# Optimization experiments

Measured on AMD Instinct MI355X. Metric: run time of the kernel, lower is better.

The kernel has to match this reference:

```python
import jax, jax.numpy as jnp
import numpy as np

H = 4      # attention heads
C = 64     # hidden_dim per head
GAT_SLOPE = 0.2   # PyG GATConv leaky_relu negative_slope
ACT_SLOPE = 0.01  # nn.LeakyReLU / F.leaky_relu default


def gat_layer(x, src, dst, W, a_src, a_dst, b, n):
    # x: [n, F_in] -> h: [n, H, C]
    h = (x @ W).reshape(n, H, C)
    al_s = jnp.einsum('nhc,hc->nh', h, a_src)  # [n, H]
    al_d = jnp.einsum('nhc,hc->nh', h, a_dst)
    e = jax.nn.leaky_relu(al_s[src] + al_d[dst], GAT_SLOPE)  # [E, H]
    # segment softmax over destination nodes (self-loops ensure non-empty segments)
    m = jax.ops.segment_max(e, dst, num_segments=n)
    p = jnp.exp(e - m[dst])
    s = jax.ops.segment_sum(p, dst, num_segments=n)
    alpha = p / s[dst]
    out = jax.ops.segment_sum(h[src] * alpha[:, :, None], dst, num_segments=n)  # [n, H, C]
    return out.reshape(n, H * C) + b


def setup_inputs() -> dict:
    key = jax.random.key(0)
    ks = jax.random.split(key, 24)
    N, E = 102400, 409600
    F_IN, F_OUT = 80, 80
    HC = H * C
    RIN, RHID, ROUT = 60, 512, 60
    def g(k, shape, scale):
        return (jax.random.normal(k, shape, dtype=jnp.float32) * scale)
    inp = {
        'x': g(ks[0], (N, F_IN), 1.0),
        'edge_index': jax.random.randint(ks[1], (2, E), 0, N, dtype=jnp.int64),
        'root_ctx_norm': g(ks[2], (4096, RIN), 1.0),
        'W0': g(ks[3], (F_IN, HC), 0.1), 'a_src0': g(ks[4], (H, C), 0.1), 'a_dst0': g(ks[5], (H, C), 0.1), 'b0': jnp.zeros((HC,), jnp.float32),
        'W1': g(ks[6], (HC, HC), 0.06), 'a_src1': g(ks[7], (H, C), 0.1), 'a_dst1': g(ks[8], (H, C), 0.1), 'b1': jnp.zeros((HC,), jnp.float32),
        'W2': g(ks[9], (HC, HC), 0.06), 'a_src2': g(ks[10], (H, C), 0.1), 'a_dst2': g(ks[11], (H, C), 0.1), 'b2': jnp.zeros((HC,), jnp.float32),
        'fc_w': g(ks[12], (HC, F_OUT), 0.06), 'fc_b': jnp.zeros((F_OUT,), jnp.float32),
        'r_w1': g(ks[13], (RIN, RHID), 0.1), 'r_b1': jnp.zeros((RHID,), jnp.float32),
        'r_w2': g(ks[14], (RHID, RHID), 0.04), 'r_b2': jnp.zeros((RHID,), jnp.float32),
        'r_w3': g(ks[15], (RHID, ROUT), 0.04), 'r_b3': jnp.zeros((ROUT,), jnp.float32),
    }
    return inp


def reference(x, edge_index, root_ctx_norm,
              W0, a_src0, a_dst0, b0,
              W1, a_src1, a_dst1, b1,
              W2, a_src2, a_dst2, b2,
              fc_w, fc_b, r_w1, r_b1, r_w2, r_b2, r_w3, r_b3):
    n = x.shape[0]
    loops = jnp.arange(n, dtype=edge_index.dtype)
    src = jnp.concatenate([edge_index[0], loops])  # PyG add_self_loops=True
    dst = jnp.concatenate([edge_index[1], loops])
    h = gat_layer(x, src, dst, W0, a_src0, a_dst0, b0, n)
    h = jax.nn.leaky_relu(h, ACT_SLOPE)  # dropout is identity in eval
    h = gat_layer(h, src, dst, W1, a_src1, a_dst1, b1, n)
    h = jax.nn.leaky_relu(h, ACT_SLOPE)
    h = gat_layer(h, src, dst, W2, a_src2, a_dst2, b2, n)
    rot = h @ fc_w + fc_b
    r = jax.nn.leaky_relu(root_ctx_norm @ r_w1 + r_b1, ACT_SLOPE)
    r = jax.nn.leaky_relu(r @ r_w2 + r_b2, ACT_SLOPE)
    root_norm = r @ r_w3 + r_b3
    return rot, root_norm
```

## Files before the change

kernel.cpp:

```cpp
#include <hip/hip_runtime.h>
#include <hip/hip_bf16.h>


#define GAT_SLOPE 0.2f
#define ACT_SLOPE 0.01f

typedef unsigned short ushort_t;
typedef __attribute__((ext_vector_type(8))) short bf16x8;
typedef __attribute__((ext_vector_type(8))) unsigned short ushort8v;
typedef __attribute__((ext_vector_type(4))) unsigned short ushort4v;
typedef __attribute__((ext_vector_type(4))) float floatx4;

__device__ __forceinline__ float lrelu(float x, float s) {
    return fmaxf(x, s * x);
}

__device__ __forceinline__ ushort_t f2bf(float f) {
    union { float f; unsigned u; } x; x.f = f;
    unsigned r = x.u + 0x7FFF + ((x.u >> 16) & 1);
    return (ushort_t)(r >> 16);
}

__device__ __forceinline__ float bf2f(ushort_t u) {
    union { unsigned u; float f; } x; x.u = ((unsigned)u) << 16;
    return x.f;
}

__device__ __forceinline__ void gl_lds16(const ushort_t* g, ushort_t* l) {
    __builtin_amdgcn_global_load_lds(
        (const __attribute__((address_space(1))) unsigned int*)g,
        (__attribute__((address_space(3))) unsigned int*)l, 16, 0, 0);
}

__global__ void detect_fmt(const int* __restrict__ raw, int nwords, int* flag) {
    __shared__ int nz;
    if (threadIdx.x == 0) nz = 0;
    __syncthreads();
    int lim = nwords < 4096 ? nwords : 4096;
    for (int i = threadIdx.x * 2 + 1; i < lim; i += 512)
        if (raw[i] != 0) atomicAdd(&nz, 1);
    __syncthreads();
    if (threadIdx.x == 0) *flag = (nz == 0) ? 1 : 0;
}

__global__ void zero2(int* __restrict__ a, int* __restrict__ b, int n) {
    int i = blockIdx.x * blockDim.x + threadIdx.x;
    if (i < n) { a[i] = 0; b[i] = 0; }
}

__global__ void convert_count(const int* __restrict__ raw, int E,
                              const int* __restrict__ flag,
                              int* __restrict__ idx32, int* __restrict__ counts) {
    int i = blockIdx.x * blockDim.x + threadIdx.x;
    if (i >= E) return;
    int f = *flag;
    int s = f ? raw[2 * i] : raw[i];
    int d = f ? raw[2 * (E + i)] : raw[E + i];
    idx32[i] = s;
    idx32[E + i] = d;
    atomicAdd(&counts[d], 1);
}

__global__ void scan_block(const int* __restrict__ counts, int* __restrict__ inc,
                           int* __restrict__ blockSums, int N) {
    __shared__ int sh[256];
    int i = blockIdx.x * 256 + threadIdx.x;
    int v = (i < N) ? counts[i] : 0;
    sh[threadIdx.x] = v;
    __syncthreads();
    for (int off = 1; off < 256; off <<= 1) {
        int t = (threadIdx.x >= off) ? sh[threadIdx.x - off] : 0;
        __syncthreads();
        sh[threadIdx.x] += t;
        __syncthreads();
    }
    if (i < N) inc[i] = sh[threadIdx.x];
    if (threadIdx.x == 255) blockSums[blockIdx.x] = sh[255];
}

__global__ void scan_sums(int* __restrict__ blockSums, int nb, int* __restrict__ row_ptr) {
    __shared__ int sh[512];
    int v = ((int)threadIdx.x < nb) ? blockSums[threadIdx.x] : 0;
    sh[threadIdx.x] = v;
    __syncthreads();
    for (int off = 1; off < 512; off <<= 1) {
        int t = (threadIdx.x >= off) ? sh[threadIdx.x - off] : 0;
        __syncthreads();
        sh[threadIdx.x] += t;
        __syncthreads();
    }
    if ((int)threadIdx.x < nb) blockSums[threadIdx.x] = sh[threadIdx.x];
    if (threadIdx.x == 0) row_ptr[0] = 0;
}

__global__ void scan_add(const int* __restrict__ inc, const int* __restrict__ blockSums,
                         int* __restrict__ row_ptr, int N) {
    int i = blockIdx.x * 256 + threadIdx.x;
    if (i < N) row_ptr[i + 1] = inc[i] + (blockIdx.x > 0 ? blockSums[blockIdx.x - 1] : 0);
}

__global__ void edge_fill(const int* __restrict__ src, const int* __restrict__ dst, int E,
                          const int* __restrict__ row_ptr, int* __restrict__ cursor,
                          int* __restrict__ col) {
    int i = blockIdx.x * blockDim.x + threadIdx.x;
    if (i < E) {
        int d = dst[i];
        int pos = row_ptr[d] + atomicAdd(&cursor[d], 1);
        col[pos] = src[i];
    }
}

__global__ void convert_padrow(const float* __restrict__ in, ushort_t* __restrict__ out,
                               int M, int Kr, int Kp) {
    int i = blockIdx.x * blockDim.x + threadIdx.x;
    if (i >= M * Kp) return;
    int r = i / Kp, c = i - r * Kp;
    out[i] = f2bf((c < Kr) ? in[(size_t)r * Kr + c] : 0.f);
}

struct WConv { const float* in; ushort_t* out; int Kp, Kr, N, Npad, blkOff; };
struct WConvArr { WConv e[7]; int n; };

__global__ void convert_w_multi(WConvArr a) {
    int b = blockIdx.x;
    int ei = 0;
    for (int k = 1; k < a.n; k++)
        if (b >= a.e[k].blkOff) ei = k;
    WConv w = a.e[ei];
    int i = (b - w.blkOff) * 256 + threadIdx.x;
    if (i >= w.Npad * w.Kp) return;
    int n = i / w.Kp, k = i - n * w.Kp;
    float v = (n < w.N && k < w.Kr) ? w.in[(size_t)k * w.N + n] : 0.f;
    w.out[i] = f2bf(v);
}

__global__ __launch_bounds__(256) void gemm_gat(
    const ushort_t* __restrict__ A, const ushort_t* __restrict__ Bt,
    const float* __restrict__ a_src, const float* __restrict__ a_dst,
    ushort_t* __restrict__ Hbf, float* __restrict__ al_s, float* __restrict__ al_d,
    int M, int K) {
    __shared__ __align__(16) ushort_t As[128 * 32];
    __shared__ __align__(16) ushort_t Bs[128 * 32];
    int t = threadIdx.x;
    int wave = t >> 6, lane = t & 63;
    int wm = (wave >> 1) << 6;
    int wn = (wave & 1) << 6;
    int rowBase = blockIdx.y << 7;
    int colBase = blockIdx.x << 7;
    int lrow = lane & 15, lquad = lane >> 4;
    floatx4 acc[4][4];
#pragma unroll
    for (int i = 0; i < 4; i++)
#pragma unroll
        for (int j = 0; j < 4; j++) acc[i][j] = (floatx4){0.f, 0.f, 0.f, 0.f};

    int c0 = wave * 64 + lane;
    const ushort_t* gA0 = A + (size_t)(rowBase + (c0 >> 2)) * K + ((c0 & 3) << 3);
    const ushort_t* gB0 = Bt + (size_t)(colBase + (c0 >> 2)) * K + ((c0 & 3) << 3);
    int c1 = 256 + c0;
    const ushort_t* gA1 = A + (size_t)(rowBase + (c1 >> 2)) * K + ((c1 & 3) << 3);
    const ushort_t* gB1 = Bt + (size_t)(colBase + (c1 >> 2)) * K + ((c1 & 3) << 3);
    ushort_t* lA0 = As + (size_t)(wave * 64) * 8;
    ushort_t* lB0 = Bs + (size_t)(wave * 64) * 8;
    ushort_t* lA1 = As + (size_t)(256 + wave * 64) * 8;
    ushort_t* lB1 = Bs + (size_t)(256 + wave * 64) * 8;

    for (int k0 = 0; k0 < K; k0 += 32) {
        gl_lds16(gA0 + k0, lA0);
        gl_lds16(gA1 + k0, lA1);
        gl_lds16(gB0 + k0, lB0);
        gl_lds16(gB1 + k0, lB1);
        __syncthreads();
        bf16x8 af[4], bfv[4];
#pragma unroll
        for (int i = 0; i < 4; i++)
            af[i] = *(const bf16x8*)(As + (wm + i * 16 + lrow) * 32 + lquad * 8);
#pragma unroll
        for (int j = 0; j < 4; j++)
            bfv[j] = *(const bf16x8*)(Bs + (wn + j * 16 + lrow) * 32 + lquad * 8);
#pragma unroll
        for (int i = 0; i < 4; i++)
#pragma unroll
            for (int j = 0; j < 4; j++)
                acc[i][j] = __builtin_amdgcn_mfma_f32_16x16x32_bf16(af[i], bfv[j],
                                                                    acc[i][j], 0, 0, 0);
        __syncthreads();
    }
    int head = (colBase + wn) >> 6;
    float avs[4], avd[4];
#pragma unroll
    for (int j = 0; j < 4; j++) {
        avs[j] = a_src[head * 64 + j * 16 + lrow];
        avd[j] = a_dst[head * 64 + j * 16 + lrow];
    }
#pragma unroll
    for (int i = 0; i < 4; i++) {
#pragma unroll
        for (int r = 0; r < 4; r++) {
            float ps = 0.f, pd = 0.f;
#pragma unroll
            for (int j = 0; j < 4; j++) {
                ps += acc[i][j][r] * avs[j];
                pd += acc[i][j][r] * avd[j];
            }
#pragma unroll
            for (int off = 1; off < 16; off <<= 1) {
                ps += __shfl_xor(ps, off);
                pd += __shfl_xor(pd, off);
            }
            if (lrow == 0) {
                int gr = rowBase + wm + i * 16 + lquad * 4 + r;
                al_s[gr * 4 + head] = ps;
                al_d[gr * 4 + head] = pd;
            }
        }
        int grb = rowBase + wm + i * 16 + lquad * 4;
#pragma unroll
        for (int j = 0; j < 4; j++) {
            int gc = colBase + wn + j * 16 + lrow;
#pragma unroll
            for (int r = 0; r < 4; r++)
                Hbf[(size_t)(grb + r) * 256 + gc] = f2bf(acc[i][j][r]);
        }
    }
}

__global__ __launch_bounds__(256) void gemm_plain(
    const ushort_t* __restrict__ A, const ushort_t* __restrict__ Bt,
    const float* __restrict__ bias, void* __restrict__ Cout,
    int M, int N, int K, int act, float slope, int outBf) {
    __shared__ __align__(16) ushort_t As[128 * 32];
    __shared__ __align__(16) ushort_t Bs[128 * 32];
    int t = threadIdx.x;
    int wave = t >> 6, lane = t & 63;
    int wm = (wave >> 1) << 6;
    int wn = (wave & 1) << 6;
    int rowBase = blockIdx.y << 7;
    int colBase = blockIdx.x << 7;
    int lrow = lane & 15, lquad = lane >> 4;
    floatx4 acc[4][4];
#pragma unroll
    for (int i = 0; i < 4; i++)
#pragma unroll
        for (int j = 0; j < 4; j++) acc[i][j] = (floatx4){0.f, 0.f, 0.f, 0.f};

    int c0 = wave * 64 + lane;
    const ushort_t* gA0 = A + (size_t)(rowBase + (c0 >> 2)) * K + ((c0 & 3) << 3);
    const ushort_t* gB0 = Bt + (size_t)(colBase + (c0 >> 2)) * K + ((c0 & 3) << 3);
    int c1 = 256 + c0;
    const ushort_t* gA1 = A + (size_t)(rowBase + (c1 >> 2)) * K + ((c1 & 3) << 3);
    const ushort_t* gB1 = Bt + (size_t)(colBase + (c1 >> 2)) * K + ((c1 & 3) << 3);
    ushort_t* lA0 = As + (size_t)(wave * 64) * 8;
    ushort_t* lB0 = Bs + (size_t)(wave * 64) * 8;
    ushort_t* lA1 = As + (size_t)(256 + wave * 64) * 8;
    ushort_t* lB1 = Bs + (size_t)(256 + wave * 64) * 8;

    for (int k0 = 0; k0 < K; k0 += 32) {
        gl_lds16(gA0 + k0, lA0);
        gl_lds16(gA1 + k0, lA1);
        gl_lds16(gB0 + k0, lB0);
        gl_lds16(gB1 + k0, lB1);
        __syncthreads();
        bf16x8 af[4], bfv[4];
#pragma unroll
        for (int i = 0; i < 4; i++)
            af[i] = *(const bf16x8*)(As + (wm + i * 16 + lrow) * 32 + lquad * 8);
#pragma unroll
        for (int j = 0; j < 4; j++)
            bfv[j] = *(const bf16x8*)(Bs + (wn + j * 16 + lrow) * 32 + lquad * 8);
#pragma unroll
        for (int i = 0; i < 4; i++)
#pragma unroll
            for (int j = 0; j < 4; j++)
                acc[i][j] = __builtin_amdgcn_mfma_f32_16x16x32_bf16(af[i], bfv[j],
                                                                    acc[i][j], 0, 0, 0);
        __syncthreads();
    }
#pragma unroll
    for (int i = 0; i < 4; i++) {
        int gr = rowBase + wm + i * 16 + lquad * 4;
#pragma unroll
        for (int j = 0; j < 4; j++) {
            int gc = colBase + wn + j * 16 + lrow;
            if (gc >= N) continue;
            float b = bias ? bias[gc] : 0.f;
#pragma unroll
            for (int r = 0; r < 4; r++) {
                float v = acc[i][j][r] + b;
                if (act) v = lrelu(v, slope);
                if (outBf)
                    ((ushort_t*)Cout)[(size_t)(gr + r) * N + gc] = f2bf(v);
                else
                    ((float*)Cout)[(size_t)(gr + r) * N + gc] = v;
            }
        }
    }
}

__global__ __launch_bounds__(256) void gat_agg(
    const ushort_t* __restrict__ h_bf, const float* __restrict__ al_s,
    const float* __restrict__ al_d, const int* __restrict__ row_ptr,
    const int* __restrict__ col, const float* __restrict__ bias,
    ushort_t* __restrict__ out_bf, int N, int act, float slope) {
    int wid = (blockIdx.x * 256 + threadIdx.x) >> 6;
    int lane = threadIdx.x & 63;
    int half = lane >> 5;
    int lane8 = lane & 31;
    int n = wid * 2 + half;
    if (n >= N) return;
    int head = lane8 >> 3;
    int idx4 = n * 4 + head;
    float ad = al_d[idx4];
    const ushort8v* h8 = (const ushort8v*)h_bf;
    float p = __expf(lrelu(al_s[idx4] + ad, GAT_SLOPE));
    ushort8v hv = h8[(size_t)n * 32 + lane8];
    float s = p;
    float acc[8];
#pragma unroll
    for (int c = 0; c < 8; c++) acc[c] = p * bf2f(hv[c]);
    int beg = row_ptr[n], end = row_ptr[n + 1];
    for (int i = beg; i < end; i += 4) {
        int cnt = end - i;
        int sn0 = col[i];
        int sn1 = (cnt > 1) ? col[i + 1] : sn0;
        int sn2 = (cnt > 2) ? col[i + 2] : sn0;
        int sn3 = (cnt > 3) ? col[i + 3] : sn0;
        ushort8v h0 = h8[(size_t)sn0 * 32 + lane8];
        ushort8v h1 = h8[(size_t)sn1 * 32 + lane8];
        ushort8v h2 = h8[(size_t)sn2 * 32 + lane8];
        ushort8v h3 = h8[(size_t)sn3 * 32 + lane8];
        float a0 = al_s[sn0 * 4 + head];
        float a1 = al_s[sn1 * 4 + head];
        float a2 = al_s[sn2 * 4 + head];
        float a3 = al_s[sn3 * 4 + head];
        float p0 = __expf(lrelu(a0 + ad, GAT_SLOPE));
#pragma unroll
        for (int c = 0; c < 8; c++) acc[c] += p0 * bf2f(h0[c]);
        s += p0;
        if (cnt > 1) {
            float p1 = __expf(lrelu(a1 + ad, GAT_SLOPE));
#pragma unroll
            for (int c = 0; c < 8; c++) acc[c] += p1 * bf2f(h1[c]);
            s += p1;
        }
        if (cnt > 2) {
            float p2 = __expf(lrelu(a2 + ad, GAT_SLOPE));
#pragma unroll
            for (int c = 0; c < 8; c++) acc[c] += p2 * bf2f(h2[c]);
            s += p2;
        }
        if (cnt > 3) {
            float p3 = __expf(lrelu(a3 + ad, GAT_SLOPE));
#pragma unroll
            for (int c = 0; c < 8; c++) acc[c] += p3 * bf2f(h3[c]);
            s += p3;
        }
    }
    float rs = 1.f / s;
    const float4* b4 = (const float4*)bias;
    float4 b0 = b4[lane8 * 2];
    float4 b1 = b4[lane8 * 2 + 1];
    float bv[8] = {b0.x, b0.y, b0.z, b0.w, b1.x, b1.y, b1.z, b1.w};
    ushort8v o;
#pragma unroll
    for (int c = 0; c < 8; c++) {
        float v = acc[c] * rs + bv[c];
        if (act) v = lrelu(v, slope);
        o[c] = f2bf(v);
    }
    ((ushort8v*)out_bf)[(size_t)n * 32 + lane8] = o;
}

extern "C" void kernel_launch(void* const* d_in, const int* in_sizes, int n_in,
                              void* d_out, int out_size, void* d_ws, size_t ws_size,
                              hipStream_t stream) {
    const float* x        = (const float*)d_in[0];
    const int*   rawEdge  = (const int*)d_in[1];
    const float* rootCtx  = (const float*)d_in[2];
    const float* W[3]     = {(const float*)d_in[3], (const float*)d_in[7], (const float*)d_in[11]};
    const float* aS[3]    = {(const float*)d_in[4], (const float*)d_in[8], (const float*)d_in[12]};
    const float* aD[3]    = {(const float*)d_in[5], (const float*)d_in[9], (const float*)d_in[13]};
    const float* bb[3]    = {(const float*)d_in[6], (const float*)d_in[10], (const float*)d_in[14]};
    const float* fc_w     = (const float*)d_in[15];
    const float* fc_b     = (const float*)d_in[16];
    const float* r_w1     = (const float*)d_in[17];
    const float* r_b1     = (const float*)d_in[18];
    const float* r_w2     = (const float*)d_in[19];
    const float* r_b2     = (const float*)d_in[20];
    const float* r_w3     = (const float*)d_in[21];
    const float* r_b3     = (const float*)d_in[22];

    const int N  = in_sizes[0] / 80;
    const int E  = in_sizes[1] / 2;
    const int R  = in_sizes[2] / 60;
    const int N4 = N * 4;

    float* outRot  = (float*)d_out;
    float* outRoot = (float*)d_out + (size_t)N * 80;

    size_t off = 0;
    auto carve = [&](size_t bytes) -> void* {
        off = (off + 255) & ~(size_t)255;
        void* p = (char*)d_ws + off;
        off += bytes;
        return p;
    };
    int*      flag      = (int*)carve(4);
    int*      idx32     = (int*)carve((size_t)2 * E * 4);
    int*      counts    = (int*)carve((size_t)N * 4);
    int*      cursor    = (int*)carve((size_t)N * 4);
    int*      row_ptr   = (int*)carve((size_t)(N + 1) * 4);
    int*      incArr    = (int*)carve((size_t)N * 4);
    int*      blockSums = (int*)carve(512 * 4);
    int*      colArr    = (int*)carve((size_t)E * 4);
    float*    al_s      = (float*)carve((size_t)N4 * 4);
    float*    al_d      = (float*)carve((size_t)N4 * 4);
    ushort_t* h_bf      = (ushort_t*)carve((size_t)N * 256 * 2);
    ushort_t* agg_bf    = (ushort_t*)carve((size_t)N * 256 * 2);
    ushort_t* x_bf      = (ushort_t*)carve((size_t)N * 96 * 2);
    ushort_t* rc_bf     = (ushort_t*)carve((size_t)R * 64 * 2);
    ushort_t* t1_bf     = (ushort_t*)carve((size_t)R * 512 * 2);
    ushort_t* t2_bf     = (ushort_t*)carve((size_t)R * 512 * 2);
    ushort_t* Wt0       = (ushort_t*)carve((size_t)256 * 96 * 2);
    ushort_t* Wt1       = (ushort_t*)carve((size_t)256 * 256 * 2);
    ushort_t* Wt2       = (ushort_t*)carve((size_t)256 * 256 * 2);
    ushort_t* fcWt      = (ushort_t*)carve((size_t)128 * 256 * 2);
    ushort_t* rW1t      = (ushort_t*)carve((size_t)512 * 64 * 2);
    ushort_t* rWt2      = (ushort_t*)carve((size_t)512 * 512 * 2);
    ushort_t* rWt3      = (ushort_t*)carve((size_t)128 * 512 * 2);

    const int nb = (N + 255) / 256;
    dim3 blk(256);

    detect_fmt<<<1, 256, 0, stream>>>(rawEdge, 2 * E, flag);
    zero2<<<(N + 255) / 256, blk, 0, stream>>>(counts, cursor, N);
    convert_count<<<(E + 255) / 256, blk, 0, stream>>>(rawEdge, E, flag, idx32, counts);
    const int* srcArr = idx32;
    const int* dstArr = idx32 + E;
    scan_block<<<nb, 256, 0, stream>>>(counts, incArr, blockSums, N);
    scan_sums<<<1, 512, 0, stream>>>(blockSums, nb, row_ptr);
    scan_add<<<nb, 256, 0, stream>>>(incArr, blockSums, row_ptr, N);
    edge_fill<<<(E + 255) / 256, blk, 0, stream>>>(srcArr, dstArr, E, row_ptr, cursor, colArr);

    {
        WConvArr wa;
        auto mk = [&](int i, const float* in, ushort_t* out, int Kp, int Kr, int Nn, int Npad,
                      int blkOff) {
            wa.e[i] = WConv{in, out, Kp, Kr, Nn, Npad, blkOff};
        };
        int boff = 0;
        auto nblk = [](int Npad, int Kp) { return (Npad * Kp + 255) / 256; };
        mk(0, W[0], Wt0, 96, 80, 256, 256, boff);   boff += nblk(256, 96);
        mk(1, W[1], Wt1, 256, 256, 256, 256, boff); boff += nblk(256, 256);
        mk(2, W[2], Wt2, 256, 256, 256, 256, boff); boff += nblk(256, 256);
        mk(3, fc_w, fcWt, 256, 256, 80, 128, boff); boff += nblk(128, 256);
        mk(4, r_w1, rW1t, 64, 60, 512, 512, boff);  boff += nblk(512, 64);
        mk(5, r_w2, rWt2, 512, 512, 512, 512, boff); boff += nblk(512, 512);
        mk(6, r_w3, rWt3, 512, 512, 60, 128, boff);  boff += nblk(128, 512);
        wa.n = 7;
        convert_w_multi<<<boff, blk, 0, stream>>>(wa);
    }
    convert_padrow<<<(N * 96 + 255) / 256, blk, 0, stream>>>(x, x_bf, N, 80, 96);
    convert_padrow<<<(R * 64 + 255) / 256, blk, 0, stream>>>(rootCtx, rc_bf, R, 60, 64);

    const int aggBlocks = (N / 2 + 3) / 4;
    const ushort_t* curA = x_bf;
    int curK = 96;
    for (int l = 0; l < 3; l++) {
        dim3 g1(2, N / 128);
        gemm_gat<<<g1, blk, 0, stream>>>(curA, l == 0 ? Wt0 : (l == 1 ? Wt1 : Wt2),
                                         aS[l], aD[l], h_bf, al_s, al_d, N, curK);
        int act = (l < 2) ? 1 : 0;
        gat_agg<<<aggBlocks, blk, 0, stream>>>(h_bf, al_s, al_d, row_ptr,
                                               colArr, bb[l], agg_bf, N,
                                               act, ACT_SLOPE);
        curA = agg_bf;
        curK = 256;
    }

    {
        dim3 g(1, N / 128);
        gemm_plain<<<g, blk, 0, stream>>>(agg_bf, fcWt, fc_b, outRot, N, 80, 256,
                                          0, 0.f, 0);
    }
    {
        dim3 g1(512 / 128, R / 128);
        gemm_plain<<<g1, blk, 0, stream>>>(rc_bf, rW1t, r_b1, t1_bf, R, 512, 64,
                                           1, ACT_SLOPE, 1);
        dim3 g2(512 / 128, R / 128);
        gemm_plain<<<g2, blk, 0, stream>>>(t1_bf, rWt2, r_b2, t2_bf, R, 512, 512,
                                           1, ACT_SLOPE, 1);
        dim3 g3(1, R / 128);
        gemm_plain<<<g3, blk, 0, stream>>>(t2_bf, rWt3, r_b3, outRoot, R, 60, 512,
                                           0, 0.f, 0);
    }
}
```

Measured before the change: 520.8 us.

## Double-buffer LDS tiles in both GEMM kernels to overlap loads with MFMA

```diff
diff --git a/kernel.cpp b/kernel.cpp
--- a/kernel.cpp
+++ b/kernel.cpp
@@ -139,8 +139,8 @@
     const float* __restrict__ a_src, const float* __restrict__ a_dst,
     ushort_t* __restrict__ Hbf, float* __restrict__ al_s, float* __restrict__ al_d,
     int M, int K) {
-    __shared__ __align__(16) ushort_t As[128 * 32];
-    __shared__ __align__(16) ushort_t Bs[128 * 32];
+    __shared__ __align__(16) ushort_t As[2][128 * 32];
+    __shared__ __align__(16) ushort_t Bs[2][128 * 32];
     int t = threadIdx.x;
     int wave = t >> 6, lane = t & 63;
     int wm = (wave >> 1) << 6;
@@ -160,32 +160,53 @@
     int c1 = 256 + c0;
     const ushort_t* gA1 = A + (size_t)(rowBase + (c1 >> 2)) * K + ((c1 & 3) << 3);
     const ushort_t* gB1 = Bt + (size_t)(colBase + (c1 >> 2)) * K + ((c1 & 3) << 3);
-    ushort_t* lA0 = As + (size_t)(wave * 64) * 8;
-    ushort_t* lB0 = Bs + (size_t)(wave * 64) * 8;
-    ushort_t* lA1 = As + (size_t)(256 + wave * 64) * 8;
-    ushort_t* lB1 = Bs + (size_t)(256 + wave * 64) * 8;
-
-    for (int k0 = 0; k0 < K; k0 += 32) {
-        gl_lds16(gA0 + k0, lA0);
-        gl_lds16(gA1 + k0, lA1);
-        gl_lds16(gB0 + k0, lB0);
-        gl_lds16(gB1 + k0, lB1);
-        __syncthreads();
+    const int ldsOff0 = (wave * 64) * 8;
+    const int ldsOff1 = (256 + wave * 64) * 8;
+
+    const int nt = K >> 5;
+#define STAGE_GAT(tt, b)                          \
+    do {                                          \
+        int k0_ = (tt) << 5;                      \
+        gl_lds16(gA0 + k0_, &As[b][ldsOff0]);     \
+        gl_lds16(gA1 + k0_, &As[b][ldsOff1]);     \
+        gl_lds16(gB0 + k0_, &Bs[b][ldsOff0]);     \
+        gl_lds16(gB1 + k0_, &Bs[b][ldsOff1]);     \
+    } while (0)
+
+    STAGE_GAT(0, 0);
+    STAGE_GAT(1, 1);
+    asm volatile("s_waitcnt vmcnt(4)" ::: "memory");
+    __builtin_amdgcn_s_barrier();
+
+    for (int kt = 0; kt < nt; ++kt) {
+        int b = kt & 1;
         bf16x8 af[4], bfv[4];
 #pragma unroll
         for (int i = 0; i < 4; i++)
-            af[i] = *(const bf16x8*)(As + (wm + i * 16 + lrow) * 32 + lquad * 8);
+            af[i] = *(const bf16x8*)(&As[b][(wm + i * 16 + lrow) * 32 + lquad * 8]);
 #pragma unroll
         for (int j = 0; j < 4; j++)
-            bfv[j] = *(const bf16x8*)(Bs + (wn + j * 16 + lrow) * 32 + lquad * 8);
+            bfv[j] = *(const bf16x8*)(&Bs[b][(wn + j * 16 + lrow) * 32 + lquad * 8]);
+        asm volatile("s_waitcnt lgkmcnt(0)" ::: "memory");
+        __builtin_amdgcn_sched_barrier(0);
+        __builtin_amdgcn_s_barrier();
+        bool more = (kt + 2) < nt;
+        if (more) STAGE_GAT(kt + 2, b);
 #pragma unroll
         for (int i = 0; i < 4; i++)
 #pragma unroll
             for (int j = 0; j < 4; j++)
                 acc[i][j] = __builtin_amdgcn_mfma_f32_16x16x32_bf16(af[i], bfv[j],
                                                                     acc[i][j], 0, 0, 0);
-        __syncthreads();
-    }
+        if (more)
+            asm volatile("s_waitcnt vmcnt(4)" ::: "memory");
+        else
+            asm volatile("s_waitcnt vmcnt(0)" ::: "memory");
+        __builtin_amdgcn_s_barrier();
+        __builtin_amdgcn_sched_barrier(0);
+    }
+#undef STAGE_GAT
+
     int head = (colBase + wn) >> 6;
     float avs[4], avd[4];
 #pragma unroll
@@ -229,8 +250,8 @@
     const ushort_t* __restrict__ A, const ushort_t* __restrict__ Bt,
     const float* __restrict__ bias, void* __restrict__ Cout,
     int M, int N, int K, int act, float slope, int outBf) {
-    __shared__ __align__(16) ushort_t As[128 * 32];
-    __shared__ __align__(16) ushort_t Bs[128 * 32];
+    __shared__ __align__(16) ushort_t As[2][128 * 32];
+    __shared__ __align__(16) ushort_t Bs[2][128 * 32];
     int t = threadIdx.x;
     int wave = t >> 6, lane = t & 63;
     int wm = (wave >> 1) << 6;
@@ -250,32 +271,53 @@
     int c1 = 256 + c0;
     const ushort_t* gA1 = A + (size_t)(rowBase + (c1 >> 2)) * K + ((c1 & 3) << 3);
     const ushort_t* gB1 = Bt + (size_t)(colBase + (c1 >> 2)) * K + ((c1 & 3) << 3);
-    ushort_t* lA0 = As + (size_t)(wave * 64) * 8;
-    ushort_t* lB0 = Bs + (size_t)(wave * 64) * 8;
-    ushort_t* lA1 = As + (size_t)(256 + wave * 64) * 8;
-    ushort_t* lB1 = Bs + (size_t)(256 + wave * 64) * 8;
-
-    for (int k0 = 0; k0 < K; k0 += 32) {
-        gl_lds16(gA0 + k0, lA0);
-        gl_lds16(gA1 + k0, lA1);
-        gl_lds16(gB0 + k0, lB0);
-        gl_lds16(gB1 + k0, lB1);
-        __syncthreads();
+    const int ldsOff0 = (wave * 64) * 8;
+    const int ldsOff1 = (256 + wave * 64) * 8;
+
+    const int nt = K >> 5;
+#define STAGE_PLN(tt, b)                          \
+    do {                                          \
+        int k0_ = (tt) << 5;                      \
+        gl_lds16(gA0 + k0_, &As[b][ldsOff0]);     \
+        gl_lds16(gA1 + k0_, &As[b][ldsOff1]);     \
+        gl_lds16(gB0 + k0_, &Bs[b][ldsOff0]);     \
+        gl_lds16(gB1 + k0_, &Bs[b][ldsOff1]);     \
+    } while (0)
+
+    STAGE_PLN(0, 0);
+    STAGE_PLN(1, 1);
+    asm volatile("s_waitcnt vmcnt(4)" ::: "memory");
+    __builtin_amdgcn_s_barrier();
+
+    for (int kt = 0; kt < nt; ++kt) {
+        int b = kt & 1;
         bf16x8 af[4], bfv[4];
 #pragma unroll
         for (int i = 0; i < 4; i++)
-            af[i] = *(const bf16x8*)(As + (wm + i * 16 + lrow) * 32 + lquad * 8);
+            af[i] = *(const bf16x8*)(&As[b][(wm + i * 16 + lrow) * 32 + lquad * 8]);
 #pragma unroll
         for (int j = 0; j < 4; j++)
-            bfv[j] = *(const bf16x8*)(Bs + (wn + j * 16 + lrow) * 32 + lquad * 8);
+            bfv[j] = *(const bf16x8*)(&Bs[b][(wn + j * 16 + lrow) * 32 + lquad * 8]);
+        asm volatile("s_waitcnt lgkmcnt(0)" ::: "memory");
+        __builtin_amdgcn_sched_barrier(0);
+        __builtin_amdgcn_s_barrier();
+        bool more = (kt + 2) < nt;
+        if (more) STAGE_PLN(kt + 2, b);
 #pragma unroll
         for (int i = 0; i < 4; i++)
 #pragma unroll
             for (int j = 0; j < 4; j++)
                 acc[i][j] = __builtin_amdgcn_mfma_f32_16x16x32_bf16(af[i], bfv[j],
                                                                     acc[i][j], 0, 0, 0);
-        __syncthreads();
-    }
+        if (more)
+            asm volatile("s_waitcnt vmcnt(4)" ::: "memory");
+        else
+            asm volatile("s_waitcnt vmcnt(0)" ::: "memory");
+        __builtin_amdgcn_s_barrier();
+        __builtin_amdgcn_sched_barrier(0);
+    }
+#undef STAGE_PLN
+
 #pragma unroll
     for (int i = 0; i < 4; i++) {
         int gr = rowBase + wm + i * 16 + lquad * 4;
```

After: 514.8 us. Within noise of the previous version (-1.2%).

## Double-buffer GEMM tiles with register-staged prefetch and 64-wide K steps

Applied to the files above, without the earlier changes.

```diff
diff --git a/kernel.cpp b/kernel.cpp
--- a/kernel.cpp
+++ b/kernel.cpp
@@ -8,7 +8,6 @@
 typedef unsigned short ushort_t;
 typedef __attribute__((ext_vector_type(8))) short bf16x8;
 typedef __attribute__((ext_vector_type(8))) unsigned short ushort8v;
-typedef __attribute__((ext_vector_type(4))) unsigned short ushort4v;
 typedef __attribute__((ext_vector_type(4))) float floatx4;
 
 __device__ __forceinline__ float lrelu(float x, float s) {
@@ -24,12 +23,6 @@
 __device__ __forceinline__ float bf2f(ushort_t u) {
     union { unsigned u; float f; } x; x.u = ((unsigned)u) << 16;
     return x.f;
-}
-
-__device__ __forceinline__ void gl_lds16(const ushort_t* g, ushort_t* l) {
-    __builtin_amdgcn_global_load_lds(
-        (const __attribute__((address_space(1))) unsigned int*)g,
-        (__attribute__((address_space(3))) unsigned int*)l, 16, 0, 0);
 }
 
 __global__ void detect_fmt(const int* __restrict__ raw, int nwords, int* flag) {
@@ -134,13 +127,60 @@
     w.out[i] = f2bf(v);
 }
 
+#define DECL_P()                                      \
+    ushort8v pa0, pa1, pb0, pb1, qa0, qa1, qb0, qb1
+
+#define LOADP(pp)                                     \
+    do {                                              \
+        int k0_ = (pp) << 6;                          \
+        pa0 = *(const ushort8v*)(gA0 + k0_);          \
+        pa1 = *(const ushort8v*)(gA1 + k0_);          \
+        pb0 = *(const ushort8v*)(gB0 + k0_);          \
+        pb1 = *(const ushort8v*)(gB1 + k0_);          \
+        qa0 = *(const ushort8v*)(gA0 + k0_ + 32);     \
+        qa1 = *(const ushort8v*)(gA1 + k0_ + 32);     \
+        qb0 = *(const ushort8v*)(gB0 + k0_ + 32);     \
+        qb1 = *(const ushort8v*)(gB1 + k0_ + 32);     \
+    } while (0)
+
+#define WRITEP(b)                                     \
+    do {                                              \
+        *(ushort8v*)(&As[b][wsl0]) = pa0;             \
+        *(ushort8v*)(&As[b][wsl1]) = pa1;             \
+        *(ushort8v*)(&Bs[b][wsl0]) = pb0;             \
+        *(ushort8v*)(&Bs[b][wsl1]) = pb1;             \
+        *(ushort8v*)(&As[b][4096 + wsl0]) = qa0;      \
+        *(ushort8v*)(&As[b][4096 + wsl1]) = qa1;      \
+        *(ushort8v*)(&Bs[b][4096 + wsl0]) = qb0;      \
+        *(ushort8v*)(&Bs[b][4096 + wsl1]) = qb1;      \
+    } while (0)
+
+#define MFMA_SUB(b, base)                                                        \
+    do {                                                                         \
+        bf16x8 af[4], bfv[4];                                                    \
+        _Pragma("unroll")                                                        \
+        for (int i = 0; i < 4; i++)                                              \
+            af[i] = *(const bf16x8*)(&As[b][(base) + (wm + i * 16 + lrow) * 32   \
+                                            + lquad * 8]);                       \
+        _Pragma("unroll")                                                        \
+        for (int j = 0; j < 4; j++)                                              \
+            bfv[j] = *(const bf16x8*)(&Bs[b][(base) + (wn + j * 16 + lrow) * 32  \
+                                             + lquad * 8]);                      \
+        _Pragma("unroll")                                                        \
+        for (int i = 0; i < 4; i++)                                              \
+            _Pragma("unroll")                                                    \
+            for (int j = 0; j < 4; j++)                                          \
+                acc[i][j] = __builtin_amdgcn_mfma_f32_16x16x32_bf16(             \
+                    af[i], bfv[j], acc[i][j], 0, 0, 0);                          \
+    } while (0)
+
 __global__ __launch_bounds__(256) void gemm_gat(
     const ushort_t* __restrict__ A, const ushort_t* __restrict__ Bt,
     const float* __restrict__ a_src, const float* __restrict__ a_dst,
     ushort_t* __restrict__ Hbf, float* __restrict__ al_s, float* __restrict__ al_d,
     int M, int K) {
-    __shared__ __align__(16) ushort_t As[128 * 32];
-    __shared__ __align__(16) ushort_t Bs[128 * 32];
+    __shared__ __align__(16) ushort_t As[2][128 * 64];
+    __shared__ __align__(16) ushort_t Bs[2][128 * 64];
     int t = threadIdx.x;
     int wave = t >> 6, lane = t & 63;
     int wm = (wave >> 1) << 6;
@@ -160,32 +200,28 @@
     int c1 = 256 + c0;
     const ushort_t* gA1 = A + (size_t)(rowBase + (c1 >> 2)) * K + ((c1 & 3) << 3);
     const ushort_t* gB1 = Bt + (size_t)(colBase + (c1 >> 2)) * K + ((c1 & 3) << 3);
-    ushort_t* lA0 = As + (size_t)(wave * 64) * 8;
-    ushort_t* lB0 = Bs + (size_t)(wave * 64) * 8;
-    ushort_t* lA1 = As + (size_t)(256 + wave * 64) * 8;
-    ushort_t* lB1 = Bs + (size_t)(256 + wave * 64) * 8;
-
-    for (int k0 = 0; k0 < K; k0 += 32) {
-        gl_lds16(gA0 + k0, lA0);
-        gl_lds16(gA1 + k0, lA1);
-        gl_lds16(gB0 + k0, lB0);
-        gl_lds16(gB1 + k0, lB1);
-        __syncthreads();
-        bf16x8 af[4], bfv[4];
-#pragma unroll
-        for (int i = 0; i < 4; i++)
-            af[i] = *(const bf16x8*)(As + (wm + i * 16 + lrow) * 32 + lquad * 8);
-#pragma unroll
-        for (int j = 0; j < 4; j++)
-            bfv[j] = *(const bf16x8*)(Bs + (wn + j * 16 + lrow) * 32 + lquad * 8);
-#pragma unroll
-        for (int i = 0; i < 4; i++)
-#pragma unroll
-            for (int j = 0; j < 4; j++)
-                acc[i][j] = __builtin_amdgcn_mfma_f32_16x16x32_bf16(af[i], bfv[j],
-                                                                    acc[i][j], 0, 0, 0);
-        __syncthreads();
-    }
+    const int wsl0 = (wave * 64 + lane) * 8;
+    const int wsl1 = (256 + wave * 64 + lane) * 8;
+
+    const int np = K >> 6;
+    DECL_P();
+
+    LOADP(0);
+    WRITEP(0);
+    if (np > 1) LOADP(1);
+    asm volatile("s_waitcnt lgkmcnt(0)" ::: "memory");
+    __builtin_amdgcn_s_barrier();
+
+    for (int kp = 0; kp < np; ++kp) {
+        int b = kp & 1;
+        if (kp + 1 < np) WRITEP(b ^ 1);
+        if (kp + 2 < np) LOADP(kp + 2);
+        MFMA_SUB(b, 0);
+        MFMA_SUB(b, 4096);
+        asm volatile("s_waitcnt lgkmcnt(0)" ::: "memory");
+        __builtin_amdgcn_s_barrier();
+    }
+
     int head = (colBase + wn) >> 6;
     float avs[4], avd[4];
 #pragma unroll
@@ -229,8 +265,8 @@
     const ushort_t* __restrict__ A, const ushort_t* __restrict__ Bt,
     const float* __restrict__ bias, void* __restrict__ Cout,
     int M, int N, int K, int act, float slope, int outBf) {
-    __shared__ __align__(16) ushort_t As[128 * 32];
-    __shared__ __align__(16) ushort_t Bs[128 * 32];
+    __shared__ __align__(16) ushort_t As[2][128 * 64];
+    __shared__ __align__(16) ushort_t Bs[2][128 * 64];
     int t = threadIdx.x;
     int wave = t >> 6, lane = t & 63;
     int wm = (wave >> 1) << 6;
@@ -250,32 +286,28 @@
     int c1 = 256 + c0;
     const ushort_t* gA1 = A + (size_t)(rowBase + (c1 >> 2)) * K + ((c1 & 3) << 3);
     const ushort_t* gB1 = Bt + (size_t)(colBase + (c1 >> 2)) * K + ((c1 & 3) << 3);
-    ushort_t* lA0 = As + (size_t)(wave * 64) * 8;
-    ushort_t* lB0 = Bs + (size_t)(wave * 64) * 8;
-    ushort_t* lA1 = As + (size_t)(256 + wave * 64) * 8;
-    ushort_t* lB1 = Bs + (size_t)(256 + wave * 64) * 8;
-
-    for (int k0 = 0; k0 < K; k0 += 32) {
-        gl_lds16(gA0 + k0, lA0);
-        gl_lds16(gA1 + k0, lA1);
-        gl_lds16(gB0 + k0, lB0);
-        gl_lds16(gB1 + k0, lB1);
-        __syncthreads();
-        bf16x8 af[4], bfv[4];
-#pragma unroll
-        for (int i = 0; i < 4; i++)
-            af[i] = *(const bf16x8*)(As + (wm + i * 16 + lrow) * 32 + lquad * 8);
-#pragma unroll
-        for (int j = 0; j < 4; j++)
-            bfv[j] = *(const bf16x8*)(Bs + (wn + j * 16 + lrow) * 32 + lquad * 8);
-#pragma unroll
-        for (int i = 0; i < 4; i++)
-#pragma unroll
-            for (int j = 0; j < 4; j++)
-                acc[i][j] = __builtin_amdgcn_mfma_f32_16x16x32_bf16(af[i], bfv[j],
-                                                                    acc[i][j], 0, 0, 0);
-        __syncthreads();
-    }
+    const int wsl0 = (wave * 64 + lane) * 8;
+    const int wsl1 = (256 + wave * 64 + lane) * 8;
+
+    const int np = K >> 6;
+    DECL_P();
+
+    LOADP(0);
+    WRITEP(0);
+    if (np > 1) LOADP(1);
+    asm volatile("s_waitcnt lgkmcnt(0)" ::: "memory");
+    __builtin_amdgcn_s_barrier();
+
+    for (int kp = 0; kp < np; ++kp) {
+        int b = kp & 1;
+        if (kp + 1 < np) WRITEP(b ^ 1);
+        if (kp + 2 < np) LOADP(kp + 2);
+        MFMA_SUB(b, 0);
+        MFMA_SUB(b, 4096);
+        asm volatile("s_waitcnt lgkmcnt(0)" ::: "memory");
+        __builtin_amdgcn_s_barrier();
+    }
+
 #pragma unroll
     for (int i = 0; i < 4; i++) {
         int gr = rowBase + wm + i * 16 + lquad * 4;
@@ -417,11 +449,11 @@
     float*    al_d      = (float*)carve((size_t)N4 * 4);
     ushort_t* h_bf      = (ushort_t*)carve((size_t)N * 256 * 2);
     ushort_t* agg_bf    = (ushort_t*)carve((size_t)N * 256 * 2);
-    ushort_t* x_bf      = (ushort_t*)carve((size_t)N * 96 * 2);
+    ushort_t* x_bf      = (ushort_t*)carve((size_t)N * 128 * 2);
     ushort_t* rc_bf     = (ushort_t*)carve((size_t)R * 64 * 2);
     ushort_t* t1_bf     = (ushort_t*)carve((size_t)R * 512 * 2);
     ushort_t* t2_bf     = (ushort_t*)carve((size_t)R * 512 * 2);
-    ushort_t* Wt0       = (ushort_t*)carve((size_t)256 * 96 * 2);
+    ushort_t* Wt0       = (ushort_t*)carve((size_t)256 * 128 * 2);
     ushort_t* Wt1       = (ushort_t*)carve((size_t)256 * 256 * 2);
     ushort_t* Wt2       = (ushort_t*)carve((size_t)256 * 256 * 2);
     ushort_t* fcWt      = (ushort_t*)carve((size_t)128 * 256 * 2);
@@ -450,7 +482,7 @@
         };
         int boff = 0;
         auto nblk = [](int Npad, int Kp) { return (Npad * Kp + 255) / 256; };
-        mk(0, W[0], Wt0, 96, 80, 256, 256, boff);   boff += nblk(256, 96);
+        mk(0, W[0], Wt0, 128, 80, 256, 256, boff);  boff += nblk(256, 128);
         mk(1, W[1], Wt1, 256, 256, 256, 256, boff); boff += nblk(256, 256);
         mk(2, W[2], Wt2, 256, 256, 256, 256, boff); boff += nblk(256, 256);
         mk(3, fc_w, fcWt, 256, 256, 80, 128, boff); boff += nblk(128, 256);
@@ -460,12 +492,12 @@
         wa.n = 7;
         convert_w_multi<<<boff, blk, 0, stream>>>(wa);
     }
-    convert_padrow<<<(N * 96 + 255) / 256, blk, 0, stream>>>(x, x_bf, N, 80, 96);
+    convert_padrow<<<(N * 128 + 255) / 256, blk, 0, stream>>>(x, x_bf, N, 80, 128);
     convert_padrow<<<(R * 64 + 255) / 256, blk, 0, stream>>>(rootCtx, rc_bf, R, 60, 64);
 
     const int aggBlocks = (N / 2 + 3) / 4;
     const ushort_t* curA = x_bf;
-    int curK = 96;
+    int curK = 128;
     for (int l = 0; l < 3; l++) {
         dim3 g1(2, N / 128);
         gemm_gat<<<g1, blk, 0, stream>>>(curA, l == 0 ? Wt0 : (l == 1 ? Wt1 : Wt2),
```

Result: no change. 521.3 us (+0.1%).
